# Optimization experiments

Measured on AMD Instinct MI355X. Metric: run time of the kernel, lower is better.

## Reference

```python
import jax, jax.numpy as jnp
import numpy as np

NUM_ITERS = 3
NUM_SLOTS = 8
D = 128
MLP_HIDDEN = 128
EPS = 1e-8
LN_EPS = 1e-5
B, N = 64, 4096


def _layer_norm(x, g, b):
    m = jnp.mean(x, axis=-1, keepdims=True)
    v = jnp.mean(jnp.square(x - m), axis=-1, keepdims=True)
    return (x - m) * jax.lax.rsqrt(v + LN_EPS) * g + b


def setup_inputs() -> dict:
    key = jax.random.key(0)
    ks = jax.random.split(key, 16)
    s = 1.0 / np.sqrt(D)
    inp = {
        "x": jax.random.normal(ks[0], (B, N, D), jnp.float32),
        "slots_init": jax.random.normal(ks[1], (B, NUM_SLOTS, D), jnp.float32),
        "Wq": jax.random.normal(ks[2], (D, D), jnp.float32) * s,
        "bq": jnp.zeros((D,), jnp.float32),
        "Wk": jax.random.normal(ks[3], (D, D), jnp.float32) * s,
        "bk": jnp.zeros((D,), jnp.float32),
        "Wv": jax.random.normal(ks[4], (D, D), jnp.float32) * s,
        "bv": jnp.zeros((D,), jnp.float32),
        "g_in": jnp.ones((D,), jnp.float32), "b_in": jnp.zeros((D,), jnp.float32),
        "g_slot": jnp.ones((D,), jnp.float32), "b_slot": jnp.zeros((D,), jnp.float32),
        "g_mlp": jnp.ones((D,), jnp.float32), "b_mlp": jnp.zeros((D,), jnp.float32),
        "W1": jax.random.normal(ks[5], (MLP_HIDDEN, D), jnp.float32) * s,
        "b1": jnp.zeros((MLP_HIDDEN,), jnp.float32),
        "W2": jax.random.normal(ks[6], (D, MLP_HIDDEN), jnp.float32) * (1.0 / np.sqrt(MLP_HIDDEN)),
        "b2": jnp.zeros((D,), jnp.float32),
        "W_ih": jax.random.normal(ks[7], (3 * D, D), jnp.float32) * s,
        "W_hh": jax.random.normal(ks[8], (3 * D, D), jnp.float32) * s,
        "b_ih": jnp.zeros((3 * D,), jnp.float32),
        "b_hh": jnp.zeros((3 * D,), jnp.float32),
    }
    return inp


def _gru_cell(x, h, W_ih, W_hh, b_ih, b_hh):
    # torch.nn.GRUCell semantics
    gi = x @ W_ih.T + b_ih          # [.., 3D]
    gh = h @ W_hh.T + b_hh
    i_r, i_z, i_n = jnp.split(gi, 3, axis=-1)
    h_r, h_z, h_n = jnp.split(gh, 3, axis=-1)
    r = jax.nn.sigmoid(i_r + h_r)
    z = jax.nn.sigmoid(i_z + h_z)
    n = jnp.tanh(i_n + r * h_n)
    return (1.0 - z) * n + z * h


def reference(x, slots_init, Wq, bq, Wk, bk, Wv, bv, g_in, b_in, g_slot, b_slot,
              g_mlp, b_mlp, W1, b1, W2, b2, W_ih, W_hh, b_ih, b_hh):
    xn = _layer_norm(x, g_in, b_in)                 # [B,N,D]
    keys = xn @ Wk.T + bk                            # [B,N,D]
    values = xn @ Wv.T + bv                          # [B,N,D]
    scale = D ** -0.5
    slots = slots_init                               # [B,K,D]
    for _ in range(NUM_ITERS):
        prev = slots
        s = _layer_norm(slots, g_slot, b_slot)
        q = s @ Wq.T + bq                            # [B,K,D]
        logits = jnp.einsum('bid,bkd->bik', q, keys) * scale  # [B,K,N]
        attn = jax.nn.softmax(logits, axis=1)        # softmax over SLOT axis
        attn = attn + EPS
        attn = attn / jnp.sum(attn, axis=-1, keepdims=True)
        updates = jnp.einsum('bkd,bik->bid', values, attn)     # [B,K,D]
        slots = _gru_cell(updates.reshape(-1, D), prev.reshape(-1, D),
                          W_ih, W_hh, b_ih, b_hh).reshape(x.shape[0], -1, D)
        h = jax.nn.relu(_layer_norm(slots, g_mlp, b_mlp) @ W1.T + b1)
        slots = slots + (h @ W2.T + b2)
    return slots
```

## Files before the change

### kernel.cpp

```cpp
#include <hip/hip_runtime.h>
#include <hip/hip_bf16.h>

#define B_ 64
#define N_ 4096
#define KS 8
#define NCH 64
#define TP 136
#define LNEPS 1e-5f
#define EPSA 1e-8f
#define SCALE 0.08838834764831845f

typedef short short8  __attribute__((ext_vector_type(8)));
typedef short short4v __attribute__((ext_vector_type(4)));
typedef float f32x4   __attribute__((ext_vector_type(4)));

__device__ __forceinline__ unsigned short f2bf(float f) {
  union { float f; unsigned u; } v; v.f = f;
  unsigned r = v.u + 0x7fffu + ((v.u >> 16) & 1u);
  return (unsigned short)(r >> 16);
}
__device__ __forceinline__ float bflo(unsigned u) {
  union { unsigned u; float f; } c; c.u = u << 16; return c.f;
}
__device__ __forceinline__ float bfhi(unsigned u) {
  union { unsigned u; float f; } c; c.u = u & 0xffff0000u; return c.f;
}
__device__ __forceinline__ float sigmf(float x) { return 1.f / (1.f + __expf(-x)); }

__global__ __launch_bounds__(256) void prep_weights(
    const float* __restrict__ Wih, const float* __restrict__ Whh,
    const float* __restrict__ Wq,  const float* __restrict__ Wv,
    const float* __restrict__ W1,  const float* __restrict__ W2,
    float* __restrict__ WgT, float* __restrict__ WqT,
    float* __restrict__ WvT, float* __restrict__ W1T, float* __restrict__ W2T)
{
  int id = blockIdx.x * 256 + threadIdx.x;
  if (id < 98304) {
    int d = id / 768, j = id % 768;
    WgT[id] = (j < 384) ? Wih[j*128 + d] : Whh[(j-384)*128 + d];
  } else if (id < 114688) {
    int k = id - 98304; WqT[k] = Wq[(k % 128) * 128 + k / 128];
  } else if (id < 131072) {
    int k = id - 114688; WvT[k] = Wv[(k % 128) * 128 + k / 128];
  } else if (id < 147456) {
    int k = id - 131072; W1T[k] = W1[(k % 128) * 128 + k / 128];
  } else if (id < 163840) {
    int k = id - 147456; W2T[k] = W2[(k % 128) * 128 + k / 128];
  }
}

__global__ __launch_bounds__(256) void q_init_kernel(
    const float* __restrict__ slots_in, const float* __restrict__ g_slot, const float* __restrict__ b_slot,
    const float* __restrict__ WqT, const float* __restrict__ bq,
    const float* __restrict__ Wk, const float* __restrict__ bk,
    float* __restrict__ qt, float* __restrict__ qc)
{
  __shared__ float sarr[128];
  __shared__ float qarr[128];
  int row = blockIdx.x, t = threadIdx.x;
  if (t < 64) {
    float a = slots_in[row*128 + t], b = slots_in[row*128 + 64 + t];
    float s = a + b, s2 = a*a + b*b;
    #pragma unroll
    for (int st = 1; st < 64; st <<= 1) { s += __shfl_xor(s, st); s2 += __shfl_xor(s2, st); }
    float mean = s * (1.f/128.f);
    float rstd = rsqrtf(s2 * (1.f/128.f) - mean*mean + LNEPS);
    sarr[t]    = (a - mean) * rstd * g_slot[t]    + b_slot[t];
    sarr[t+64] = (b - mean) * rstd * g_slot[t+64] + b_slot[t+64];
  }
  __syncthreads();
  if (t < 128) {
    float a = bq[t];
    for (int d = 0; d < 128; d++) a += sarr[d] * WqT[d*128 + t];
    qarr[t] = a;
  }
  __syncthreads();
  if (t < 128) {
    float a = 0.f;
    for (int j = 0; j < 128; j++) a += qarr[j] * Wk[j*128 + t];
    qt[row*128 + t] = a * SCALE;
  }
  if (t < 64) {
    float c = qarr[t]*bk[t] + qarr[t+64]*bk[t+64];
    #pragma unroll
    for (int st = 1; st < 64; st <<= 1) c += __shfl_xor(c, st);
    if (t == 0) qc[row] = c * SCALE;
  }
}

template<bool FUSE_LN>
__global__ __launch_bounds__(256) void attn_kernel(
    const float* __restrict__ x, const float* __restrict__ g_in, const float* __restrict__ b_in,
    unsigned short* __restrict__ xn,
    const float* __restrict__ qt, const float* __restrict__ qc,
    float* __restrict__ Upart, float* __restrict__ Spart)
{
  __shared__ union ShMem {
    unsigned short xt[4][16][TP];
    float ured[4][8][128];
  } sh;
  __shared__ __align__(16) float pb[4][16][8];
  __shared__ float sred[4][8];

  const int tid = threadIdx.x;
  const int w = tid >> 6, lane = tid & 63;
  const int chunk = blockIdx.x, batch = blockIdx.y;
  const int m = lane & 15, quad = lane >> 4;
  const int tb = (chunk*4 + w)*16;

  short8 afrag[4];
  if (m < KS) {
    const float* qp = qt + (batch*KS + m)*128 + quad*8;
    #pragma unroll
    for (int kc = 0; kc < 4; kc++) {
      short8 a;
      #pragma unroll
      for (int j = 0; j < 8; j++) a[j] = (short)f2bf(qp[kc*32 + j]);
      afrag[kc] = a;
    }
  } else {
    #pragma unroll
    for (int kc = 0; kc < 4; kc++) {
      short8 a;
      #pragma unroll
      for (int j = 0; j < 8; j++) a[j] = 0;
      afrag[kc] = a;
    }
  }
  float creg[4];
  #pragma unroll
  for (int r = 0; r < 4; r++) creg[r] = qc[batch*KS + ((quad*4 + r) & 7)];

  short8 bfrag[4];
  if (FUSE_LN) {
    const int rw = lane >> 2, cp = lane & 3;
    const float* xrow = x + (size_t)(batch*N_ + tb + rw) * 128;
    float4 v[8];
    float s = 0.f, s2 = 0.f;
    #pragma unroll
    for (int i = 0; i < 8; i++) {
      v[i] = *(const float4*)(xrow + (cp + 4*i)*4);
      s  += v[i].x + v[i].y + v[i].z + v[i].w;
      s2 += v[i].x*v[i].x + v[i].y*v[i].y + v[i].z*v[i].z + v[i].w*v[i].w;
    }
    s += __shfl_xor(s, 1); s2 += __shfl_xor(s2, 1);
    s += __shfl_xor(s, 2); s2 += __shfl_xor(s2, 2);
    float mean = s * (1.f/128.f);
    float rstd = rsqrtf(s2 * (1.f/128.f) - mean*mean + LNEPS);
    #pragma unroll
    for (int i = 0; i < 8; i++) {
      int col = (cp + 4*i)*4;
      float4 gg = *(const float4*)(g_in + col);
      float4 bb = *(const float4*)(b_in + col);
      short4v pk;
      pk[0] = (short)f2bf((v[i].x - mean)*rstd*gg.x + bb.x);
      pk[1] = (short)f2bf((v[i].y - mean)*rstd*gg.y + bb.y);
      pk[2] = (short)f2bf((v[i].z - mean)*rstd*gg.z + bb.z);
      pk[3] = (short)f2bf((v[i].w - mean)*rstd*gg.w + bb.w);
      *(short4v*)&sh.xt[w][rw][col] = pk;
    }
    #pragma unroll
    for (int p = 0; p < 4; p++) {
      int idx = p*64 + lane; int rr = idx >> 4, c16 = idx & 15;
      int4 dv = *(const int4*)&sh.xt[w][rr][c16*8];
      *(int4*)(xn + (size_t)(batch*N_ + tb + rr)*128 + c16*8) = dv;
    }
    #pragma unroll
    for (int kc = 0; kc < 4; kc++)
      bfrag[kc] = *(const short8*)&sh.xt[w][m][kc*32 + quad*8];
  } else {
    const unsigned short* xp = xn + (size_t)(batch*N_ + tb + m)*128;
    #pragma unroll
    for (int kc = 0; kc < 4; kc++) {
      bfrag[kc] = *(const short8*)(xp + kc*32 + quad*8);
      *(short8*)&sh.xt[w][m][kc*32 + quad*8] = bfrag[kc];
    }
  }

  f32x4 acc = {0.f, 0.f, 0.f, 0.f};
  #pragma unroll
  for (int kc = 0; kc < 4; kc++)
    acc = __builtin_amdgcn_mfma_f32_16x16x32_bf16(afrag[kc], bfrag[kc], acc, 0, 0, 0);
  float l[4], o[4];
  #pragma unroll
  for (int r = 0; r < 4; r++) l[r] = acc[r] + creg[r];
  #pragma unroll
  for (int r = 0; r < 4; r++) o[r] = __shfl_xor(l[r], 16);
  float mx = fmaxf(fmaxf(fmaxf(l[0], l[1]), fmaxf(l[2], l[3])),
                   fmaxf(fmaxf(o[0], o[1]), fmaxf(o[2], o[3])));
  float e0 = __expf(l[0]-mx), e1 = __expf(l[1]-mx), e2 = __expf(l[2]-mx), e3 = __expf(l[3]-mx);
  float den = e0+e1+e2+e3 + __expf(o[0]-mx)+__expf(o[1]-mx)+__expf(o[2]-mx)+__expf(o[3]-mx);
  float rd = 1.f / den;
  float p0 = e0*rd + EPSA, p1 = e1*rd + EPSA, p2 = e2*rd + EPSA, p3 = e3*rd + EPSA;
  float sac[4] = {p0, p1, p2, p3};
  if (lane < 32) {
    float4 pv; pv.x = p0; pv.y = p1; pv.z = p2; pv.w = p3;
    *(float4*)&pb[w][m][quad*4] = pv;
  }

  float u0[8], u1[8];
  #pragma unroll
  for (int i = 0; i < 8; i++) { u0[i] = 0.f; u1[i] = 0.f; }
  #pragma unroll
  for (int t = 0; t < 16; t++) {
    float4 pA = *(const float4*)&pb[w][t][0];
    float4 pB = *(const float4*)&pb[w][t][4];
    unsigned vp = *(const unsigned*)&sh.xt[w][t][lane*2];
    float f0 = bflo(vp), f1 = bfhi(vp);
    u0[0] += pA.x*f0; u1[0] += pA.x*f1;
    u0[1] += pA.y*f0; u1[1] += pA.y*f1;
    u0[2] += pA.z*f0; u1[2] += pA.z*f1;
    u0[3] += pA.w*f0; u1[3] += pA.w*f1;
    u0[4] += pB.x*f0; u1[4] += pB.x*f1;
    u0[5] += pB.y*f0; u1[5] += pB.y*f1;
    u0[6] += pB.z*f0; u1[6] += pB.z*f1;
    u0[7] += pB.w*f0; u1[7] += pB.w*f1;
  }

  #pragma unroll
  for (int st = 1; st < 16; st <<= 1) {
    #pragma unroll
    for (int r = 0; r < 4; r++) sac[r] += __shfl_xor(sac[r], st);
  }
  if (lane == 0)  { sred[w][0]=sac[0]; sred[w][1]=sac[1]; sred[w][2]=sac[2]; sred[w][3]=sac[3]; }
  if (lane == 16) { sred[w][4]=sac[0]; sred[w][5]=sac[1]; sred[w][6]=sac[2]; sred[w][7]=sac[3]; }

  __syncthreads();
  #pragma unroll
  for (int i = 0; i < 8; i++)
    *(float2*)&sh.ured[w][i][lane*2] = make_float2(u0[i], u1[i]);
  __syncthreads();

  {
    const float* ur = &sh.ured[0][0][0];
    int i4 = tid * 4;
    float4 a = *(const float4*)(ur + i4);
    float4 b = *(const float4*)(ur + 1024 + i4);
    float4 c = *(const float4*)(ur + 2048 + i4);
    float4 d = *(const float4*)(ur + 3072 + i4);
    float4 o4;
    o4.x = a.x+b.x+c.x+d.x; o4.y = a.y+b.y+c.y+d.y;
    o4.z = a.z+b.z+c.z+d.z; o4.w = a.w+b.w+c.w+d.w;
    *(float4*)(Upart + (size_t)(batch*NCH + chunk)*1024 + i4) = o4;
    if (tid < 8)
      Spart[(batch*NCH + chunk)*8 + tid] =
        sred[0][tid] + sred[1][tid] + sred[2][tid] + sred[3][tid];
  }
}

__global__ __launch_bounds__(256) void update_kernel(
    const float* __restrict__ slots_in, float* __restrict__ slots_out,
    const float* __restrict__ Upart, const float* __restrict__ Spart,
    const float* __restrict__ WvT, const float* __restrict__ bv,
    const float* __restrict__ WgT,
    const float* __restrict__ b_ih, const float* __restrict__ b_hh,
    const float* __restrict__ g_mlp, const float* __restrict__ b_mlp,
    const float* __restrict__ W1T, const float* __restrict__ b1,
    const float* __restrict__ W2T, const float* __restrict__ b2,
    const float* __restrict__ g_slot, const float* __restrict__ b_slot,
    const float* __restrict__ WqT, const float* __restrict__ bq,
    const float* __restrict__ Wk, const float* __restrict__ bk,
    float* __restrict__ qt, float* __restrict__ qc)
{
  __shared__ float bu[128], su[128], hb[128];
  __shared__ float gg[768];
  __shared__ float s1[128], smv[128], hmv[128], s2v[128], sqv[128], qa[128];
  __shared__ float up2[2][128];
  __shared__ float stats[2], sSum;
  int row = blockIdx.x, t = threadIdx.x;
  int batch = row >> 3, slot = row & 7;

  {
    int d = t & 127, h = t >> 7;
    const float* Up = Upart + ((size_t)(batch*NCH + h*32)*8 + slot)*128 + d;
    float ua = 0.f;
    #pragma unroll 8
    for (int c = 0; c < 32; c++) ua += Up[(size_t)c*1024];
    up2[h][d] = ua;
  }
  if (t < 64) {
    float sv = Spart[(batch*NCH + t)*8 + slot];
    #pragma unroll
    for (int st = 1; st < 64; st <<= 1) sv += __shfl_xor(sv, st);
    if (t == 0) sSum = sv;
  }
  if (t >= 64 && t < 192) hb[t-64] = slots_in[row*128 + (t-64)];
  __syncthreads();
  if (t < 128) bu[t] = (up2[0][t] + up2[1][t]) / sSum;
  __syncthreads();
  if (t < 128) {
    float a = bv[t];
    for (int d = 0; d < 128; d++) a += bu[d] * WvT[d*128 + t];
    su[t] = a;
  }
  __syncthreads();
  {
    float a0 = b_ih[t];
    float a1 = (t < 128) ? b_ih[256+t] : b_hh[t-128];
    float a2 = b_hh[t+128];
    const float* v1p = (t < 128) ? su : hb;
    for (int d = 0; d < 128; d++) {
      float sd = su[d], hd = hb[d], vd = v1p[d];
      const float* wr = WgT + d*768 + t;
      a0 += sd * wr[0];
      a1 += vd * wr[256];
      a2 += hd * wr[512];
    }
    gg[t] = a0; gg[t+256] = a1; gg[t+512] = a2;
  }
  __syncthreads();
  if (t < 128) {
    float r = sigmf(gg[t] + gg[384+t]);
    float z = sigmf(gg[128+t] + gg[512+t]);
    float n = tanhf(gg[256+t] + r * gg[640+t]);
    s1[t] = (1.f - z)*n + z*hb[t];
  }
  __syncthreads();
  if (t < 64) {
    float a = s1[t], b = s1[t+64];
    float s = a + b, s2 = a*a + b*b;
    #pragma unroll
    for (int st = 1; st < 64; st <<= 1) { s += __shfl_xor(s, st); s2 += __shfl_xor(s2, st); }
    if (t == 0) { float mean = s*(1.f/128.f); stats[0] = mean;
                  stats[1] = rsqrtf(s2*(1.f/128.f) - mean*mean + LNEPS); }
  }
  __syncthreads();
  if (t < 128) smv[t] = (s1[t] - stats[0])*stats[1]*g_mlp[t] + b_mlp[t];
  __syncthreads();
  if (t < 128) {
    float a = b1[t];
    for (int d = 0; d < 128; d++) a += smv[d]*W1T[d*128 + t];
    hmv[t] = fmaxf(a, 0.f);
  }
  __syncthreads();
  if (t < 128) {
    float a = s1[t] + b2[t];
    for (int d = 0; d < 128; d++) a += hmv[d]*W2T[d*128 + t];
    s2v[t] = a;
    slots_out[row*128 + t] = a;
  }
  __syncthreads();
  if (t < 64) {
    float a = s2v[t], b = s2v[t+64];
    float s = a + b, s2 = a*a + b*b;
    #pragma unroll
    for (int st = 1; st < 64; st <<= 1) { s += __shfl_xor(s, st); s2 += __shfl_xor(s2, st); }
    if (t == 0) { float mean = s*(1.f/128.f); stats[0] = mean;
                  stats[1] = rsqrtf(s2*(1.f/128.f) - mean*mean + LNEPS); }
  }
  __syncthreads();
  if (t < 128) sqv[t] = (s2v[t] - stats[0])*stats[1]*g_slot[t] + b_slot[t];
  __syncthreads();
  if (t < 128) {
    float a = bq[t];
    for (int d = 0; d < 128; d++) a += sqv[d]*WqT[d*128 + t];
    qa[t] = a;
  }
  __syncthreads();
  if (t < 128) {
    float a = 0.f;
    for (int j = 0; j < 128; j++) a += qa[j]*Wk[j*128 + t];
    qt[row*128 + t] = a * SCALE;
  }
  if (t < 64) {
    float c = qa[t]*bk[t] + qa[t+64]*bk[t+64];
    #pragma unroll
    for (int st = 1; st < 64; st <<= 1) c += __shfl_xor(c, st);
    if (t == 0) qc[row] = c * SCALE;
  }
}

extern "C" void kernel_launch(void* const* d_in, const int* in_sizes, int n_in,
                              void* d_out, int out_size, void* d_ws, size_t ws_size,
                              hipStream_t stream) {
  const float* x          = (const float*)d_in[0];
  const float* slots_init = (const float*)d_in[1];
  const float* Wq   = (const float*)d_in[2];
  const float* bq   = (const float*)d_in[3];
  const float* Wk   = (const float*)d_in[4];
  const float* bk   = (const float*)d_in[5];
  const float* Wv   = (const float*)d_in[6];
  const float* bv   = (const float*)d_in[7];
  const float* g_in = (const float*)d_in[8];
  const float* b_in = (const float*)d_in[9];
  const float* g_slot = (const float*)d_in[10];
  const float* b_slot = (const float*)d_in[11];
  const float* g_mlp  = (const float*)d_in[12];
  const float* b_mlp  = (const float*)d_in[13];
  const float* W1   = (const float*)d_in[14];
  const float* b1   = (const float*)d_in[15];
  const float* W2   = (const float*)d_in[16];
  const float* b2   = (const float*)d_in[17];
  const float* Wih  = (const float*)d_in[18];
  const float* Whh  = (const float*)d_in[19];
  const float* b_ih = (const float*)d_in[20];
  const float* b_hh = (const float*)d_in[21];

  char* p = (char*)d_ws;
  unsigned short* xn = (unsigned short*)p; p += (size_t)B_*N_*128*2;
  float* qt    = (float*)p; p += (size_t)B_*KS*128*4;
  float* qc    = (float*)p; p += (size_t)B_*KS*4 + 2048;
  float* slots = (float*)p; p += (size_t)B_*KS*128*4;
  float* Upart = (float*)p; p += (size_t)B_*NCH*KS*128*4;
  float* Spart = (float*)p; p += (size_t)B_*NCH*KS*4 + 2048;
  float* WgT   = (float*)p; p += 98304*4;
  float* WqT   = (float*)p; p += 16384*4;
  float* WvT   = (float*)p; p += 16384*4;
  float* W1T   = (float*)p; p += 16384*4;
  float* W2T   = (float*)p; p += 16384*4;

  prep_weights<<<640, 256, 0, stream>>>(Wih, Whh, Wq, Wv, W1, W2,
                                        WgT, WqT, WvT, W1T, W2T);
  q_init_kernel<<<512, 256, 0, stream>>>(slots_init, g_slot, b_slot, WqT, bq, Wk, bk, qt, qc);

  attn_kernel<true><<<dim3(NCH, B_), 256, 0, stream>>>(x, g_in, b_in, xn, qt, qc, Upart, Spart);
  update_kernel<<<512, 256, 0, stream>>>(slots_init, slots, Upart, Spart,
      WvT, bv, WgT, b_ih, b_hh, g_mlp, b_mlp, W1T, b1, W2T, b2,
      g_slot, b_slot, WqT, bq, Wk, bk, qt, qc);

  attn_kernel<false><<<dim3(NCH, B_), 256, 0, stream>>>(x, g_in, b_in, xn, qt, qc, Upart, Spart);
  update_kernel<<<512, 256, 0, stream>>>(slots, slots, Upart, Spart,
      WvT, bv, WgT, b_ih, b_hh, g_mlp, b_mlp, W1T, b1, W2T, b2,
      g_slot, b_slot, WqT, bq, Wk, bk, qt, qc);

  attn_kernel<false><<<dim3(NCH, B_), 256, 0, stream>>>(x, g_in, b_in, xn, qt, qc, Upart, Spart);
  update_kernel<<<512, 256, 0, stream>>>(slots, (float*)d_out, Upart, Spart,
      WvT, bv, WgT, b_ih, b_hh, g_mlp, b_mlp, W1T, b1, W2T, b2,
      g_slot, b_slot, WqT, bq, Wk, bk, qt, qc);

  (void)in_sizes; (void)n_in; (void)out_size; (void)ws_size;
}
```

Measured before the change: 394.7 us.

## Fold weight products offline, split LayerNorm kernel, and loop attention over more tokens per block

```diff
diff --git a/kernel.cpp b/kernel.cpp
--- a/kernel.cpp
+++ b/kernel.cpp
@@ -4,7 +4,7 @@
 #define B_ 64
 #define N_ 4096
 #define KS 8
-#define NCH 64
+#define NCH 16
 #define TP 136
 #define LNEPS 1e-5f
 #define EPSA 1e-8f
@@ -27,71 +27,158 @@
 }
 __device__ __forceinline__ float sigmf(float x) { return 1.f / (1.f + __expf(-x)); }
 
-__global__ __launch_bounds__(256) void prep_weights(
+__global__ __launch_bounds__(256) void prep_big(
     const float* __restrict__ Wih, const float* __restrict__ Whh,
-    const float* __restrict__ Wq,  const float* __restrict__ Wv,
-    const float* __restrict__ W1,  const float* __restrict__ W2,
-    float* __restrict__ WgT, float* __restrict__ WqT,
-    float* __restrict__ WvT, float* __restrict__ W1T, float* __restrict__ W2T)
+    const float* __restrict__ Wq,  const float* __restrict__ Wk,
+    const float* __restrict__ Wv,  const float* __restrict__ W1,
+    const float* __restrict__ W2,
+    const float* __restrict__ g_slot, const float* __restrict__ g_mlp,
+    float* __restrict__ WgT, float* __restrict__ Mq,
+    float* __restrict__ W1gT, float* __restrict__ W2T)
 {
   int id = blockIdx.x * 256 + threadIdx.x;
-  if (id < 98304) {
-    int d = id / 768, j = id % 768;
-    WgT[id] = (j < 384) ? Wih[j*128 + d] : Whh[(j-384)*128 + d];
+  if (id < 49152) {
+    int j = id >> 7, d = id & 127;
+    float a = 0.f;
+    for (int k = 0; k < 128; k++) a += Wih[j*128 + k] * Wv[k*128 + d];
+    WgT[d*768 + j] = a;
+  } else if (id < 65536) {
+    int k = id - 49152; int d = k >> 7, t = k & 127;
+    float a = 0.f;
+    for (int j = 0; j < 128; j++) a += Wk[j*128 + t] * Wq[j*128 + d];
+    Mq[d*128 + t] = a * SCALE * g_slot[d];
   } else if (id < 114688) {
-    int k = id - 98304; WqT[k] = Wq[(k % 128) * 128 + k / 128];
+    int k = id - 65536; int j = k >> 7, d = k & 127;
+    WgT[d*768 + 384 + j] = Whh[j*128 + d];
   } else if (id < 131072) {
-    int k = id - 114688; WvT[k] = Wv[(k % 128) * 128 + k / 128];
+    int k = id - 114688; int t = k >> 7, d = k & 127;
+    W1gT[d*128 + t] = W1[t*128 + d] * g_mlp[d];
   } else if (id < 147456) {
-    int k = id - 131072; W1T[k] = W1[(k % 128) * 128 + k / 128];
-  } else if (id < 163840) {
-    int k = id - 147456; W2T[k] = W2[(k % 128) * 128 + k / 128];
-  }
-}
-
-__global__ __launch_bounds__(256) void q_init_kernel(
-    const float* __restrict__ slots_in, const float* __restrict__ g_slot, const float* __restrict__ b_slot,
-    const float* __restrict__ WqT, const float* __restrict__ bq,
-    const float* __restrict__ Wk, const float* __restrict__ bk,
+    int k = id - 131072; int t = k >> 7, d = k & 127;
+    W2T[d*128 + t] = W2[t*128 + d];
+  }
+}
+
+__global__ __launch_bounds__(256) void prep_small(
+    const float* __restrict__ Wq, const float* __restrict__ Wk,
+    const float* __restrict__ Wih, const float* __restrict__ W1,
+    const float* __restrict__ bq, const float* __restrict__ bk,
+    const float* __restrict__ bv, const float* __restrict__ b_ih,
+    const float* __restrict__ b_hh, const float* __restrict__ b1,
+    const float* __restrict__ b_mlp, const float* __restrict__ b_slot,
+    const float* __restrict__ g_slot,
+    float* __restrict__ cq_vec, float* __restrict__ wqcg,
+    float* __restrict__ qc0g, float* __restrict__ bg, float* __restrict__ b1f)
+{
+  __shared__ float u[128], wqcr[128];
+  int t = threadIdx.x;
+  if (t < 128) {
+    float a = bq[t];
+    for (int d = 0; d < 128; d++) a += Wq[t*128 + d] * b_slot[d];
+    u[t] = a;
+  } else {
+    int d = t - 128;
+    float a = 0.f;
+    for (int j = 0; j < 128; j++) a += Wq[j*128 + d] * bk[j];
+    wqcr[d] = a * SCALE;
+  }
+  __syncthreads();
+  if (t < 128) {
+    float a = 0.f;
+    for (int j = 0; j < 128; j++) a += Wk[j*128 + t] * u[j];
+    cq_vec[t] = a * SCALE;
+    wqcg[t] = wqcr[t] * g_slot[t];
+  } else {
+    int d = t - 128;
+    float a = b1[d];
+    for (int k = 0; k < 128; k++) a += W1[d*128 + k] * b_mlp[k];
+    b1f[d] = a;
+  }
+  if (t < 64) {
+    float v = wqcr[t]*b_slot[t] + wqcr[t+64]*b_slot[t+64]
+            + SCALE*(bq[t]*bk[t] + bq[t+64]*bk[t+64]);
+    #pragma unroll
+    for (int st = 1; st < 64; st <<= 1) v += __shfl_xor(v, st);
+    if (t == 0) *qc0g = v;
+  }
+  #pragma unroll
+  for (int p = 0; p < 3; p++) {
+    int j = t + p*256;
+    if (j < 384) {
+      float a = b_ih[j];
+      for (int k = 0; k < 128; k++) a += Wih[j*128 + k] * bv[k];
+      bg[j] = a;
+    } else if (j < 768) {
+      bg[j] = b_hh[j - 384];
+    }
+  }
+}
+
+__global__ __launch_bounds__(256) void ln_kernel(
+    const float* __restrict__ x, const float* __restrict__ g_in, const float* __restrict__ b_in,
+    unsigned short* __restrict__ xn)
+{
+  int tid = threadIdx.x;
+  int rw = tid >> 2, cp = tid & 3;
+  size_t row = (size_t)blockIdx.x * 64 + rw;
+  const float* xrow = x + row * 128;
+  float4 v[8];
+  float s = 0.f, s2 = 0.f;
+  #pragma unroll
+  for (int i = 0; i < 8; i++) {
+    v[i] = *(const float4*)(xrow + (cp + 4*i)*4);
+    s  += v[i].x + v[i].y + v[i].z + v[i].w;
+    s2 += v[i].x*v[i].x + v[i].y*v[i].y + v[i].z*v[i].z + v[i].w*v[i].w;
+  }
+  s += __shfl_xor(s, 1); s2 += __shfl_xor(s2, 1);
+  s += __shfl_xor(s, 2); s2 += __shfl_xor(s2, 2);
+  float mean = s * (1.f/128.f);
+  float rstd = rsqrtf(s2 * (1.f/128.f) - mean*mean + LNEPS);
+  #pragma unroll
+  for (int i = 0; i < 8; i++) {
+    int col = (cp + 4*i)*4;
+    float4 gg = *(const float4*)(g_in + col);
+    float4 bb = *(const float4*)(b_in + col);
+    short4v pk;
+    pk[0] = (short)f2bf((v[i].x - mean)*rstd*gg.x + bb.x);
+    pk[1] = (short)f2bf((v[i].y - mean)*rstd*gg.y + bb.y);
+    pk[2] = (short)f2bf((v[i].z - mean)*rstd*gg.z + bb.z);
+    pk[3] = (short)f2bf((v[i].w - mean)*rstd*gg.w + bb.w);
+    *(short4v*)(xn + row*128 + col) = pk;
+  }
+}
+
+__global__ __launch_bounds__(64) void q_init_kernel(
+    const float* __restrict__ slots_in, const float* __restrict__ Mq,
+    const float* __restrict__ cq_vec, const float* __restrict__ wqcg,
+    const float* __restrict__ qc0g,
     float* __restrict__ qt, float* __restrict__ qc)
 {
-  __shared__ float sarr[128];
-  __shared__ float qarr[128];
+  __shared__ float lnr[128];
   int row = blockIdx.x, t = threadIdx.x;
-  if (t < 64) {
-    float a = slots_in[row*128 + t], b = slots_in[row*128 + 64 + t];
-    float s = a + b, s2 = a*a + b*b;
-    #pragma unroll
-    for (int st = 1; st < 64; st <<= 1) { s += __shfl_xor(s, st); s2 += __shfl_xor(s2, st); }
-    float mean = s * (1.f/128.f);
-    float rstd = rsqrtf(s2 * (1.f/128.f) - mean*mean + LNEPS);
-    sarr[t]    = (a - mean) * rstd * g_slot[t]    + b_slot[t];
-    sarr[t+64] = (b - mean) * rstd * g_slot[t+64] + b_slot[t+64];
-  }
-  __syncthreads();
-  if (t < 128) {
-    float a = bq[t];
-    for (int d = 0; d < 128; d++) a += sarr[d] * WqT[d*128 + t];
-    qarr[t] = a;
-  }
-  __syncthreads();
-  if (t < 128) {
-    float a = 0.f;
-    for (int j = 0; j < 128; j++) a += qarr[j] * Wk[j*128 + t];
-    qt[row*128 + t] = a * SCALE;
-  }
-  if (t < 64) {
-    float c = qarr[t]*bk[t] + qarr[t+64]*bk[t+64];
-    #pragma unroll
-    for (int st = 1; st < 64; st <<= 1) c += __shfl_xor(c, st);
-    if (t == 0) qc[row] = c * SCALE;
-  }
-}
-
-template<bool FUSE_LN>
+  float a = slots_in[row*128 + t], b = slots_in[row*128 + 64 + t];
+  float s = a + b, s2 = a*a + b*b;
+  #pragma unroll
+  for (int st = 1; st < 64; st <<= 1) { s += __shfl_xor(s, st); s2 += __shfl_xor(s2, st); }
+  float mean = s * (1.f/128.f);
+  float rstd = rsqrtf(s2 * (1.f/128.f) - mean*mean + LNEPS);
+  lnr[t] = (a - mean)*rstd; lnr[t+64] = (b - mean)*rstd;
+  __syncthreads();
+  float a0 = cq_vec[t], a1 = cq_vec[t+64];
+  for (int d = 0; d < 128; d++) {
+    float l = lnr[d];
+    a0 += Mq[d*128 + t] * l;
+    a1 += Mq[d*128 + 64 + t] * l;
+  }
+  qt[row*128 + t] = a0; qt[row*128 + 64 + t] = a1;
+  float vq = wqcg[t]*lnr[t] + wqcg[t+64]*lnr[t+64];
+  #pragma unroll
+  for (int st = 1; st < 64; st <<= 1) vq += __shfl_xor(vq, st);
+  if (t == 0) qc[row] = vq + *qc0g;
+}
+
 __global__ __launch_bounds__(256) void attn_kernel(
-    const float* __restrict__ x, const float* __restrict__ g_in, const float* __restrict__ b_in,
-    unsigned short* __restrict__ xn,
+    const unsigned short* __restrict__ xn,
     const float* __restrict__ qt, const float* __restrict__ qc,
     float* __restrict__ Upart, float* __restrict__ Spart)
 {
@@ -106,7 +193,6 @@
   const int w = tid >> 6, lane = tid & 63;
   const int chunk = blockIdx.x, batch = blockIdx.y;
   const int m = lane & 15, quad = lane >> 4;
-  const int tb = (chunk*4 + w)*16;
 
   short8 afrag[4];
   if (m < KS) {
@@ -131,90 +217,68 @@
   #pragma unroll
   for (int r = 0; r < 4; r++) creg[r] = qc[batch*KS + ((quad*4 + r) & 7)];
 
-  short8 bfrag[4];
-  if (FUSE_LN) {
-    const int rw = lane >> 2, cp = lane & 3;
-    const float* xrow = x + (size_t)(batch*N_ + tb + rw) * 128;
-    float4 v[8];
-    float s = 0.f, s2 = 0.f;
-    #pragma unroll
-    for (int i = 0; i < 8; i++) {
-      v[i] = *(const float4*)(xrow + (cp + 4*i)*4);
-      s  += v[i].x + v[i].y + v[i].z + v[i].w;
-      s2 += v[i].x*v[i].x + v[i].y*v[i].y + v[i].z*v[i].z + v[i].w*v[i].w;
-    }
-    s += __shfl_xor(s, 1); s2 += __shfl_xor(s2, 1);
-    s += __shfl_xor(s, 2); s2 += __shfl_xor(s2, 2);
-    float mean = s * (1.f/128.f);
-    float rstd = rsqrtf(s2 * (1.f/128.f) - mean*mean + LNEPS);
-    #pragma unroll
-    for (int i = 0; i < 8; i++) {
-      int col = (cp + 4*i)*4;
-      float4 gg = *(const float4*)(g_in + col);
-      float4 bb = *(const float4*)(b_in + col);
-      short4v pk;
-      pk[0] = (short)f2bf((v[i].x - mean)*rstd*gg.x + bb.x);
-      pk[1] = (short)f2bf((v[i].y - mean)*rstd*gg.y + bb.y);
-      pk[2] = (short)f2bf((v[i].z - mean)*rstd*gg.z + bb.z);
-      pk[3] = (short)f2bf((v[i].w - mean)*rstd*gg.w + bb.w);
-      *(short4v*)&sh.xt[w][rw][col] = pk;
-    }
-    #pragma unroll
-    for (int p = 0; p < 4; p++) {
-      int idx = p*64 + lane; int rr = idx >> 4, c16 = idx & 15;
-      int4 dv = *(const int4*)&sh.xt[w][rr][c16*8];
-      *(int4*)(xn + (size_t)(batch*N_ + tb + rr)*128 + c16*8) = dv;
+  float u0[8], u1[8], sac[4];
+  #pragma unroll
+  for (int i = 0; i < 8; i++) { u0[i] = 0.f; u1[i] = 0.f; }
+  #pragma unroll
+  for (int r = 0; r < 4; r++) sac[r] = 0.f;
+
+  const unsigned short* xbase =
+      xn + ((size_t)batch*N_ + chunk*256 + w*64 + m)*128 + quad*8;
+
+  short8 cur[4], nxt[4];
+  #pragma unroll
+  for (int kc = 0; kc < 4; kc++) cur[kc] = *(const short8*)(xbase + kc*32);
+
+  for (int g = 0; g < 4; g++) {
+    if (g < 3) {
+      #pragma unroll
+      for (int kc = 0; kc < 4; kc++)
+        nxt[kc] = *(const short8*)(xbase + (g+1)*2048 + kc*32);
     }
     #pragma unroll
     for (int kc = 0; kc < 4; kc++)
-      bfrag[kc] = *(const short8*)&sh.xt[w][m][kc*32 + quad*8];
-  } else {
-    const unsigned short* xp = xn + (size_t)(batch*N_ + tb + m)*128;
-    #pragma unroll
-    for (int kc = 0; kc < 4; kc++) {
-      bfrag[kc] = *(const short8*)(xp + kc*32 + quad*8);
-      *(short8*)&sh.xt[w][m][kc*32 + quad*8] = bfrag[kc];
-    }
-  }
-
-  f32x4 acc = {0.f, 0.f, 0.f, 0.f};
-  #pragma unroll
-  for (int kc = 0; kc < 4; kc++)
-    acc = __builtin_amdgcn_mfma_f32_16x16x32_bf16(afrag[kc], bfrag[kc], acc, 0, 0, 0);
-  float l[4], o[4];
-  #pragma unroll
-  for (int r = 0; r < 4; r++) l[r] = acc[r] + creg[r];
-  #pragma unroll
-  for (int r = 0; r < 4; r++) o[r] = __shfl_xor(l[r], 16);
-  float mx = fmaxf(fmaxf(fmaxf(l[0], l[1]), fmaxf(l[2], l[3])),
-                   fmaxf(fmaxf(o[0], o[1]), fmaxf(o[2], o[3])));
-  float e0 = __expf(l[0]-mx), e1 = __expf(l[1]-mx), e2 = __expf(l[2]-mx), e3 = __expf(l[3]-mx);
-  float den = e0+e1+e2+e3 + __expf(o[0]-mx)+__expf(o[1]-mx)+__expf(o[2]-mx)+__expf(o[3]-mx);
-  float rd = 1.f / den;
-  float p0 = e0*rd + EPSA, p1 = e1*rd + EPSA, p2 = e2*rd + EPSA, p3 = e3*rd + EPSA;
-  float sac[4] = {p0, p1, p2, p3};
-  if (lane < 32) {
-    float4 pv; pv.x = p0; pv.y = p1; pv.z = p2; pv.w = p3;
-    *(float4*)&pb[w][m][quad*4] = pv;
-  }
-
-  float u0[8], u1[8];
-  #pragma unroll
-  for (int i = 0; i < 8; i++) { u0[i] = 0.f; u1[i] = 0.f; }
-  #pragma unroll
-  for (int t = 0; t < 16; t++) {
-    float4 pA = *(const float4*)&pb[w][t][0];
-    float4 pB = *(const float4*)&pb[w][t][4];
-    unsigned vp = *(const unsigned*)&sh.xt[w][t][lane*2];
-    float f0 = bflo(vp), f1 = bfhi(vp);
-    u0[0] += pA.x*f0; u1[0] += pA.x*f1;
-    u0[1] += pA.y*f0; u1[1] += pA.y*f1;
-    u0[2] += pA.z*f0; u1[2] += pA.z*f1;
-    u0[3] += pA.w*f0; u1[3] += pA.w*f1;
-    u0[4] += pB.x*f0; u1[4] += pB.x*f1;
-    u0[5] += pB.y*f0; u1[5] += pB.y*f1;
-    u0[6] += pB.z*f0; u1[6] += pB.z*f1;
-    u0[7] += pB.w*f0; u1[7] += pB.w*f1;
+      *(short8*)&sh.xt[w][m][kc*32 + quad*8] = cur[kc];
+
+    f32x4 acc = {0.f, 0.f, 0.f, 0.f};
+    #pragma unroll
+    for (int kc = 0; kc < 4; kc++)
+      acc = __builtin_amdgcn_mfma_f32_16x16x32_bf16(afrag[kc], cur[kc], acc, 0, 0, 0);
+
+    float l[4], o[4];
+    #pragma unroll
+    for (int r = 0; r < 4; r++) l[r] = acc[r] + creg[r];
+    #pragma unroll
+    for (int r = 0; r < 4; r++) o[r] = __shfl_xor(l[r], 16);
+    float mx = fmaxf(fmaxf(fmaxf(l[0], l[1]), fmaxf(l[2], l[3])),
+                     fmaxf(fmaxf(o[0], o[1]), fmaxf(o[2], o[3])));
+    float e0 = __expf(l[0]-mx), e1 = __expf(l[1]-mx), e2 = __expf(l[2]-mx), e3 = __expf(l[3]-mx);
+    float den = e0+e1+e2+e3 + __expf(o[0]-mx)+__expf(o[1]-mx)+__expf(o[2]-mx)+__expf(o[3]-mx);
+    float rd = 1.f / den;
+    float p0 = e0*rd + EPSA, p1 = e1*rd + EPSA, p2 = e2*rd + EPSA, p3 = e3*rd + EPSA;
+    sac[0] += p0; sac[1] += p1; sac[2] += p2; sac[3] += p3;
+    if (lane < 32) {
+      float4 pv; pv.x = p0; pv.y = p1; pv.z = p2; pv.w = p3;
+      *(float4*)&pb[w][m][quad*4] = pv;
+    }
+
+    #pragma unroll
+    for (int t = 0; t < 16; t++) {
+      float4 pA = *(const float4*)&pb[w][t][0];
+      float4 pB = *(const float4*)&pb[w][t][4];
+      unsigned vp = *(const unsigned*)&sh.xt[w][t][lane*2];
+      float f0 = bflo(vp), f1 = bfhi(vp);
+      u0[0] += pA.x*f0; u1[0] += pA.x*f1;
+      u0[1] += pA.y*f0; u1[1] += pA.y*f1;
+      u0[2] += pA.z*f0; u1[2] += pA.z*f1;
+      u0[3] += pA.w*f0; u1[3] += pA.w*f1;
+      u0[4] += pB.x*f0; u1[4] += pB.x*f1;
+      u0[5] += pB.y*f0; u1[5] += pB.y*f1;
+      u0[6] += pB.z*f0; u1[6] += pB.z*f1;
+      u0[7] += pB.w*f0; u1[7] += pB.w*f1;
+    }
+    #pragma unroll
+    for (int kc = 0; kc < 4; kc++) cur[kc] = nxt[kc];
   }
 
   #pragma unroll
@@ -251,56 +315,42 @@
 __global__ __launch_bounds__(256) void update_kernel(
     const float* __restrict__ slots_in, float* __restrict__ slots_out,
     const float* __restrict__ Upart, const float* __restrict__ Spart,
-    const float* __restrict__ WvT, const float* __restrict__ bv,
-    const float* __restrict__ WgT,
-    const float* __restrict__ b_ih, const float* __restrict__ b_hh,
-    const float* __restrict__ g_mlp, const float* __restrict__ b_mlp,
-    const float* __restrict__ W1T, const float* __restrict__ b1,
+    const float* __restrict__ WgT, const float* __restrict__ bg,
+    const float* __restrict__ W1gT, const float* __restrict__ b1f,
     const float* __restrict__ W2T, const float* __restrict__ b2,
-    const float* __restrict__ g_slot, const float* __restrict__ b_slot,
-    const float* __restrict__ WqT, const float* __restrict__ bq,
-    const float* __restrict__ Wk, const float* __restrict__ bk,
+    const float* __restrict__ Mq, const float* __restrict__ cq_vec,
+    const float* __restrict__ wqcg, const float* __restrict__ qc0g,
     float* __restrict__ qt, float* __restrict__ qc)
 {
-  __shared__ float bu[128], su[128], hb[128];
-  __shared__ float gg[768];
-  __shared__ float s1[128], smv[128], hmv[128], s2v[128], sqv[128], qa[128];
-  __shared__ float up2[2][128];
+  __shared__ float bu[128], hb[128], gg[768];
+  __shared__ float s1[128], lnr[128], hmv[128], s2v[128], lnr2[128];
   __shared__ float stats[2], sSum;
   int row = blockIdx.x, t = threadIdx.x;
   int batch = row >> 3, slot = row & 7;
 
+  float usum = 0.f;
+  if (t < 128) {
+    const float* Up = Upart + ((size_t)(batch*NCH)*8 + slot)*128 + t;
+    #pragma unroll
+    for (int c = 0; c < NCH; c++) usum += Up[(size_t)c*1024];
+  } else {
+    hb[t-128] = slots_in[row*128 + (t-128)];
+    if (t < 192) {
+      int l2 = t - 128;
+      float sv = (l2 < NCH) ? Spart[(batch*NCH + l2)*8 + slot] : 0.f;
+      #pragma unroll
+      for (int st = 1; st < 16; st <<= 1) sv += __shfl_xor(sv, st);
+      if (l2 == 0) sSum = sv;
+    }
+  }
+  __syncthreads();
+  if (t < 128) bu[t] = usum / sSum;
+  __syncthreads();
   {
-    int d = t & 127, h = t >> 7;
-    const float* Up = Upart + ((size_t)(batch*NCH + h*32)*8 + slot)*128 + d;
-    float ua = 0.f;
-    #pragma unroll 8
-    for (int c = 0; c < 32; c++) ua += Up[(size_t)c*1024];
-    up2[h][d] = ua;
-  }
-  if (t < 64) {
-    float sv = Spart[(batch*NCH + t)*8 + slot];
-    #pragma unroll
-    for (int st = 1; st < 64; st <<= 1) sv += __shfl_xor(sv, st);
-    if (t == 0) sSum = sv;
-  }
-  if (t >= 64 && t < 192) hb[t-64] = slots_in[row*128 + (t-64)];
-  __syncthreads();
-  if (t < 128) bu[t] = (up2[0][t] + up2[1][t]) / sSum;
-  __syncthreads();
-  if (t < 128) {
-    float a = bv[t];
-    for (int d = 0; d < 128; d++) a += bu[d] * WvT[d*128 + t];
-    su[t] = a;
-  }
-  __syncthreads();
-  {
-    float a0 = b_ih[t];
-    float a1 = (t < 128) ? b_ih[256+t] : b_hh[t-128];
-    float a2 = b_hh[t+128];
-    const float* v1p = (t < 128) ? su : hb;
+    float a0 = bg[t], a1 = bg[t+256], a2 = bg[t+512];
+    const float* v1p = (t < 128) ? bu : hb;
     for (int d = 0; d < 128; d++) {
-      float sd = su[d], hd = hb[d], vd = v1p[d];
+      float sd = bu[d], hd = hb[d], vd = v1p[d];
       const float* wr = WgT + d*768 + t;
       a0 += sd * wr[0];
       a1 += vd * wr[256];
@@ -325,17 +375,17 @@
                   stats[1] = rsqrtf(s2*(1.f/128.f) - mean*mean + LNEPS); }
   }
   __syncthreads();
-  if (t < 128) smv[t] = (s1[t] - stats[0])*stats[1]*g_mlp[t] + b_mlp[t];
-  __syncthreads();
-  if (t < 128) {
-    float a = b1[t];
-    for (int d = 0; d < 128; d++) a += smv[d]*W1T[d*128 + t];
+  if (t < 128) lnr[t] = (s1[t] - stats[0])*stats[1];
+  __syncthreads();
+  if (t < 128) {
+    float a = b1f[t];
+    for (int d = 0; d < 128; d++) a += W1gT[d*128 + t]*lnr[d];
     hmv[t] = fmaxf(a, 0.f);
   }
   __syncthreads();
   if (t < 128) {
     float a = s1[t] + b2[t];
-    for (int d = 0; d < 128; d++) a += hmv[d]*W2T[d*128 + t];
+    for (int d = 0; d < 128; d++) a += W2T[d*128 + t]*hmv[d];
     s2v[t] = a;
     slots_out[row*128 + t] = a;
   }
@@ -349,24 +399,18 @@
                   stats[1] = rsqrtf(s2*(1.f/128.f) - mean*mean + LNEPS); }
   }
   __syncthreads();
-  if (t < 128) sqv[t] = (s2v[t] - stats[0])*stats[1]*g_slot[t] + b_slot[t];
-  __syncthreads();
-  if (t < 128) {
-    float a = bq[t];
-    for (int d = 0; d < 128; d++) a += sqv[d]*WqT[d*128 + t];
-    qa[t] = a;
-  }
-  __syncthreads();
-  if (t < 128) {
-    float a = 0.f;
-    for (int j = 0; j < 128; j++) a += qa[j]*Wk[j*128 + t];
-    qt[row*128 + t] = a * SCALE;
+  if (t < 128) lnr2[t] = (s2v[t] - stats[0])*stats[1];
+  __syncthreads();
+  if (t < 128) {
+    float a = cq_vec[t];
+    for (int d = 0; d < 128; d++) a += Mq[d*128 + t]*lnr2[d];
+    qt[row*128 + t] = a;
   }
   if (t < 64) {
-    float c = qa[t]*bk[t] + qa[t+64]*bk[t+64];
-    #pragma unroll
-    for (int st = 1; st < 64; st <<= 1) c += __shfl_xor(c, st);
-    if (t == 0) qc[row] = c * SCALE;
+    float v = wqcg[t]*lnr2[t] + wqcg[t+64]*lnr2[t+64];
+    #pragma unroll
+    for (int st = 1; st < 64; st <<= 1) v += __shfl_xor(v, st);
+    if (t == 0) qc[row] = v + *qc0g;
   }
 }
 
@@ -399,34 +443,38 @@
   char* p = (char*)d_ws;
   unsigned short* xn = (unsigned short*)p; p += (size_t)B_*N_*128*2;
   float* qt    = (float*)p; p += (size_t)B_*KS*128*4;
-  float* qc    = (float*)p; p += (size_t)B_*KS*4 + 2048;
+  float* qc    = (float*)p; p += (size_t)B_*KS*4 + 1024;
   float* slots = (float*)p; p += (size_t)B_*KS*128*4;
   float* Upart = (float*)p; p += (size_t)B_*NCH*KS*128*4;
-  float* Spart = (float*)p; p += (size_t)B_*NCH*KS*4 + 2048;
+  float* Spart = (float*)p; p += (size_t)B_*NCH*KS*4 + 1024;
   float* WgT   = (float*)p; p += 98304*4;
-  float* WqT   = (float*)p; p += 16384*4;
-  float* WvT   = (float*)p; p += 16384*4;
-  float* W1T   = (float*)p; p += 16384*4;
+  float* Mq    = (float*)p; p += 16384*4;
+  float* W1gT  = (float*)p; p += 16384*4;
   float* W2T   = (float*)p; p += 16384*4;
-
-  prep_weights<<<640, 256, 0, stream>>>(Wih, Whh, Wq, Wv, W1, W2,
-                                        WgT, WqT, WvT, W1T, W2T);
-  q_init_kernel<<<512, 256, 0, stream>>>(slots_init, g_slot, b_slot, WqT, bq, Wk, bk, qt, qc);
-
-  attn_kernel<true><<<dim3(NCH, B_), 256, 0, stream>>>(x, g_in, b_in, xn, qt, qc, Upart, Spart);
+  float* cq_vec= (float*)p; p += 128*4;
+  float* wqcg  = (float*)p; p += 128*4;
+  float* qc0g  = (float*)p; p += 256;
+  float* bg    = (float*)p; p += 768*4;
+  float* b1f   = (float*)p; p += 128*4;
+
+  ln_kernel<<<4096, 256, 0, stream>>>(x, g_in, b_in, xn);
+  prep_big<<<576, 256, 0, stream>>>(Wih, Whh, Wq, Wk, Wv, W1, W2, g_slot, g_mlp,
+                                    WgT, Mq, W1gT, W2T);
+  prep_small<<<1, 256, 0, stream>>>(Wq, Wk, Wih, W1, bq, bk, bv, b_ih, b_hh, b1,
+                                    b_mlp, b_slot, g_slot, cq_vec, wqcg, qc0g, bg, b1f);
+  q_init_kernel<<<512, 64, 0, stream>>>(slots_init, Mq, cq_vec, wqcg, qc0g, qt, qc);
+
+  attn_kernel<<<dim3(NCH, B_), 256, 0, stream>>>(xn, qt, qc, Upart, Spart);
   update_kernel<<<512, 256, 0, stream>>>(slots_init, slots, Upart, Spart,
-      WvT, bv, WgT, b_ih, b_hh, g_mlp, b_mlp, W1T, b1, W2T, b2,
-      g_slot, b_slot, WqT, bq, Wk, bk, qt, qc);
-
-  attn_kernel<false><<<dim3(NCH, B_), 256, 0, stream>>>(x, g_in, b_in, xn, qt, qc, Upart, Spart);
+      WgT, bg, W1gT, b1f, W2T, b2, Mq, cq_vec, wqcg, qc0g, qt, qc);
+
+  attn_kernel<<<dim3(NCH, B_), 256, 0, stream>>>(xn, qt, qc, Upart, Spart);
   update_kernel<<<512, 256, 0, stream>>>(slots, slots, Upart, Spart,
-      WvT, bv, WgT, b_ih, b_hh, g_mlp, b_mlp, W1T, b1, W2T, b2,
-      g_slot, b_slot, WqT, bq, Wk, bk, qt, qc);
-
-  attn_kernel<false><<<dim3(NCH, B_), 256, 0, stream>>>(x, g_in, b_in, xn, qt, qc, Upart, Spart);
+      WgT, bg, W1gT, b1f, W2T, b2, Mq, cq_vec, wqcg, qc0g, qt, qc);
+
+  attn_kernel<<<dim3(NCH, B_), 256, 0, stream>>>(xn, qt, qc, Upart, Spart);
   update_kernel<<<512, 256, 0, stream>>>(slots, (float*)d_out, Upart, Spart,
-      WvT, bv, WgT, b_ih, b_hh, g_mlp, b_mlp, W1T, b1, W2T, b2,
-      g_slot, b_slot, WqT, bq, Wk, bk, qt, qc);
+      WgT, bg, W1gT, b1f, W2T, b2, Mq, cq_vec, wqcg, qc0g, qt, qc);
 
   (void)in_sizes; (void)n_in; (void)out_size; (void)ws_size;
 }
```

New measurement: 395.1 us. Within noise of the previous version (+0.1%).
